# Kernel optimization log

Hardware: AMD Instinct MI355X
Metric: run time of the kernel (lower is better)

Reference implementation:

```python
import jax, jax.numpy as jnp
import numpy as np

B, N, U = 2048, 512, 64  # batch_size, memory_len, unit_size


def setup_inputs() -> dict:
    key = jax.random.key(0)
    ks = jax.random.split(key, 7)
    memory = jax.random.normal(ks[0], (B, N, U), jnp.float32)
    k = jax.random.normal(ks[1], (B, U), jnp.float32)
    beta = jnp.full((1,), 5.0, jnp.float32)          # key strength > 0
    g = jax.random.uniform(ks[2], (1,), jnp.float32)  # interpolation gate in [0,1]
    s = jax.random.uniform(ks[3], (B, 3), jnp.float32)
    s = s / jnp.sum(s, axis=1, keepdims=True)         # shift distribution (positive)
    gamma = jnp.full((1,), 2.0, jnp.float32)          # sharpening > 1
    w_pre = jax.nn.softmax(jax.random.normal(ks[4], (B, N), jnp.float32), axis=1)
    e = jax.random.uniform(ks[5], (B, U), jnp.float32)  # erase gates in [0,1]
    a = jax.random.normal(ks[6], (B, U), jnp.float32)    # add vector
    return dict(memory=memory, k=k, beta=beta, g=g, s=s, gamma=gamma,
                w_pre=w_pre, e=e, a=a)


def _cosine_sim(x, y, eps=1e-8):
    # x: (B,N,U), y: (B,1,U); matches torch F.cosine_similarity clamping
    dot = jnp.sum(x * y, axis=-1)
    nx = jnp.maximum(jnp.sqrt(jnp.sum(x * x, axis=-1)), eps)
    ny = jnp.maximum(jnp.sqrt(jnp.sum(y * y, axis=-1)), eps)
    return dot / (nx * ny)


def reference(memory, k, beta, g, s, gamma, w_pre, e, a):
    # --- address ---
    sim = _cosine_sim(memory + 1e-16, k[:, None, :] + 1e-16)        # (B,N)
    wc = jax.nn.softmax(beta * sim, axis=1)                          # content weights
    wg = wc * g + (1.0 - g) * w_pre                                  # gated interpolation
    # circular pad by 1 on each side, then 3-tap grouped conv (cross-correlation)
    wg_pad = jnp.concatenate([wg[:, -1:], wg, wg[:, :1]], axis=1)    # (B,N+2)
    ws = (s[:, 0:1] * wg_pad[:, :-2]
          + s[:, 1:2] * wg_pad[:, 1:-1]
          + s[:, 2:3] * wg_pad[:, 2:])                               # (B,N)
    w = ws ** gamma                                                  # sharpen
    w = w / jnp.sum(w, axis=1, keepdims=True) + 1e-16                # (B,N)
    # --- read ---
    r = jnp.einsum('bn,bnu->bu', w, memory)                          # (B,U)
    # --- write: M' = M * (1 - w e^T) + w a^T ---
    new_mem = (memory * (1.0 - w[:, :, None] * e[:, None, :])
               + w[:, :, None] * a[:, None, :])                      # (B,N,U)
    return w, r, new_mem
```

## Files before the change

kernel.cpp:

```cpp
#include <hip/hip_runtime.h>
#include <math.h>

#define B_ 2048
#define N_ 512
#define U_ 64

__global__ __launch_bounds__(256) void ntm_kernel(
    const float* __restrict__ memory,
    const float* __restrict__ kk,
    const float* __restrict__ beta_p,
    const float* __restrict__ g_p,
    const float* __restrict__ sv,
    const float* __restrict__ gamma_p,
    const float* __restrict__ w_pre,
    const float* __restrict__ ev,
    const float* __restrict__ av,
    float* __restrict__ out_w,
    float* __restrict__ out_r,
    float* __restrict__ out_m)
{
    __shared__ float s_k[U_];
    __shared__ float s_sim[N_];
    __shared__ float s_wg[N_];
    __shared__ float s_red[256];
    __shared__ float s_rred[4 * U_];
    __shared__ float s_ny;

    const int b    = blockIdx.x;
    const int tid  = threadIdx.x;
    const int wave = tid >> 6;
    const int lane = tid & 63;
    const int sub  = lane >> 4;
    const int l16  = lane & 15;
    const int col  = l16 << 2;

    const float beta  = beta_p[0];
    const float g     = g_p[0];
    const float gamma = gamma_p[0];
    const float s0 = sv[b * 3 + 0], s1 = sv[b * 3 + 1], s2 = sv[b * 3 + 2];

    const size_t mem_base = (size_t)b * N_ * U_;

    if (tid < U_) {
        float kx = kk[b * U_ + tid] + 1e-16f;
        s_k[tid] = kx;
        float v = kx * kx;
        #pragma unroll
        for (int off = 32; off; off >>= 1) v += __shfl_xor(v, off);
        if (tid == 0) s_ny = fmaxf(sqrtf(v), 1e-8f);
    }
    __syncthreads();
    const float ny = s_ny;

    const float k0 = s_k[col + 0], k1 = s_k[col + 1], k2 = s_k[col + 2], k3 = s_k[col + 3];

    for (int n0 = 0; n0 < N_; n0 += 16) {
        const int n = n0 + (wave << 2) + sub;
        const float4 m4 = *(const float4*)(memory + mem_base + (size_t)n * U_ + col);
        const float x0 = m4.x + 1e-16f, x1 = m4.y + 1e-16f,
                    x2 = m4.z + 1e-16f, x3 = m4.w + 1e-16f;
        float dot = x0 * k0 + x1 * k1 + x2 * k2 + x3 * k3;
        float nsq = x0 * x0 + x1 * x1 + x2 * x2 + x3 * x3;
        #pragma unroll
        for (int off = 8; off; off >>= 1) {
            dot += __shfl_xor(dot, off);
            nsq += __shfl_xor(nsq, off);
        }
        if (l16 == 0) {
            const float nx = fmaxf(sqrtf(nsq), 1e-8f);
            s_sim[n] = dot / (nx * ny);
        }
    }
    __syncthreads();

    const int i0 = tid, i1 = tid + 256;
    const float t0 = beta * s_sim[i0];
    const float t1 = beta * s_sim[i1];

    s_red[tid] = fmaxf(t0, t1);
    __syncthreads();
    for (int ss = 128; ss > 0; ss >>= 1) {
        if (tid < ss) s_red[tid] = fmaxf(s_red[tid], s_red[tid + ss]);
        __syncthreads();
    }
    const float mx = s_red[0];
    __syncthreads();

    const float e0 = expf(t0 - mx);
    const float e1 = expf(t1 - mx);
    s_red[tid] = e0 + e1;
    __syncthreads();
    for (int ss = 128; ss > 0; ss >>= 1) {
        if (tid < ss) s_red[tid] += s_red[tid + ss];
        __syncthreads();
    }
    const float einv = 1.0f / s_red[0];
    __syncthreads();

    const float wp0 = w_pre[(size_t)b * N_ + i0];
    const float wp1 = w_pre[(size_t)b * N_ + i1];
    s_wg[i0] = g * (e0 * einv) + (1.0f - g) * wp0;
    s_wg[i1] = g * (e1 * einv) + (1.0f - g) * wp1;
    __syncthreads();

    float wsv0, wsv1;
    {
        int nm = (i0 + N_ - 1) & (N_ - 1), np = (i0 + 1) & (N_ - 1);
        wsv0 = powf(s0 * s_wg[nm] + s1 * s_wg[i0] + s2 * s_wg[np], gamma);
        nm = (i1 + N_ - 1) & (N_ - 1); np = (i1 + 1) & (N_ - 1);
        wsv1 = powf(s0 * s_wg[nm] + s1 * s_wg[i1] + s2 * s_wg[np], gamma);
    }
    s_red[tid] = wsv0 + wsv1;
    __syncthreads();
    for (int ss = 128; ss > 0; ss >>= 1) {
        if (tid < ss) s_red[tid] += s_red[tid + ss];
        __syncthreads();
    }
    const float winv = 1.0f / s_red[0];
    __syncthreads();

    const float w0 = wsv0 * winv + 1e-16f;
    const float w1 = wsv1 * winv + 1e-16f;
    s_sim[i0] = w0;
    s_sim[i1] = w1;
    out_w[(size_t)b * N_ + i0] = w0;
    out_w[(size_t)b * N_ + i1] = w1;
    __syncthreads();

    const float4 e4 = *(const float4*)(ev + b * U_ + col);
    const float4 a4 = *(const float4*)(av + b * U_ + col);
    float rx = 0.f, ry = 0.f, rz = 0.f, rw = 0.f;

    for (int n0 = 0; n0 < N_; n0 += 16) {
        const int n = n0 + (wave << 2) + sub;
        const size_t off = mem_base + (size_t)n * U_ + col;
        const float4 m4 = *(const float4*)(memory + off);
        const float wn = s_sim[n];
        float4 o;
        o.x = m4.x * (1.0f - wn * e4.x) + wn * a4.x;
        o.y = m4.y * (1.0f - wn * e4.y) + wn * a4.y;
        o.z = m4.z * (1.0f - wn * e4.z) + wn * a4.z;
        o.w = m4.w * (1.0f - wn * e4.w) + wn * a4.w;
        *(float4*)(out_m + off) = o;
        rx += wn * m4.x; ry += wn * m4.y; rz += wn * m4.z; rw += wn * m4.w;
    }
    rx += __shfl_xor(rx, 16); rx += __shfl_xor(rx, 32);
    ry += __shfl_xor(ry, 16); ry += __shfl_xor(ry, 32);
    rz += __shfl_xor(rz, 16); rz += __shfl_xor(rz, 32);
    rw += __shfl_xor(rw, 16); rw += __shfl_xor(rw, 32);
    if (lane < 16) {
        s_rred[wave * U_ + col + 0] = rx;
        s_rred[wave * U_ + col + 1] = ry;
        s_rred[wave * U_ + col + 2] = rz;
        s_rred[wave * U_ + col + 3] = rw;
    }
    __syncthreads();
    if (tid < U_) {
        const float rv = s_rred[tid] + s_rred[U_ + tid] + s_rred[2 * U_ + tid] + s_rred[3 * U_ + tid];
        out_r[(size_t)b * U_ + tid] = rv;
    }
}

extern "C" void kernel_launch(void* const* d_in, const int* in_sizes, int n_in,
                              void* d_out, int out_size, void* d_ws, size_t ws_size,
                              hipStream_t stream) {
    const float* memory = (const float*)d_in[0];
    const float* kk     = (const float*)d_in[1];
    const float* beta   = (const float*)d_in[2];
    const float* g      = (const float*)d_in[3];
    const float* sv     = (const float*)d_in[4];
    const float* gamma  = (const float*)d_in[5];
    const float* w_pre  = (const float*)d_in[6];
    const float* ev     = (const float*)d_in[7];
    const float* av     = (const float*)d_in[8];

    float* out   = (float*)d_out;
    float* out_w = out;
    float* out_r = out + (size_t)B_ * N_;
    float* out_m = out + (size_t)B_ * N_ + (size_t)B_ * U_;

    ntm_kernel<<<B_, 256, 0, stream>>>(memory, kk, beta, g, sv, gamma,
                                       w_pre, ev, av, out_w, out_r, out_m);
}
```

Baseline: 491.1 us.

## Stage per-batch memory tile in LDS to read HBM once

Each block now copies its whole 512x64 memory slice into LDS (128 KB) with async global_load_lds. Both the cosine-similarity pass and the read/write pass then use that copy, so memory is read from HBM once instead of twice. The block grows to 512 threads with wave-shuffle reductions, the output uses nontemporal stores, and powf/expf become fast __expf/__logf. The softmax max-subtraction is dropped. The large LDS footprint limits each CU to one block, which leaves less latency hiding, and skipping the max shift risks overflow for large beta.

```diff
diff --git a/kernel.cpp b/kernel.cpp
--- a/kernel.cpp
+++ b/kernel.cpp
@@ -5,7 +5,11 @@
 #define N_ 512
 #define U_ 64
 
-__global__ __launch_bounds__(256) void ntm_kernel(
+typedef float f4 __attribute__((ext_vector_type(4)));
+
+#define NT_STORE4(ptr, v) __builtin_nontemporal_store((v), (f4*)(ptr))
+
+__global__ __launch_bounds__(512, 1) void ntm_kernel(
     const float* __restrict__ memory,
     const float* __restrict__ kk,
     const float* __restrict__ beta_p,
@@ -19,46 +23,60 @@
     float* __restrict__ out_r,
     float* __restrict__ out_m)
 {
-    __shared__ float s_k[U_];
+    __shared__ float s_mem[N_ * U_];
     __shared__ float s_sim[N_];
     __shared__ float s_wg[N_];
-    __shared__ float s_red[256];
-    __shared__ float s_rred[4 * U_];
-    __shared__ float s_ny;
+    __shared__ float s_red[8];
+    __shared__ float s_red2[8];
+    __shared__ float s_rred[8 * U_];
 
     const int b    = blockIdx.x;
     const int tid  = threadIdx.x;
     const int wave = tid >> 6;
     const int lane = tid & 63;
-    const int sub  = lane >> 4;
-    const int l16  = lane & 15;
+    const int grp  = tid >> 4;
+    const int l16  = tid & 15;
     const int col  = l16 << 2;
+
+    const size_t mem_base = (size_t)b * N_ * U_;
 
     const float beta  = beta_p[0];
     const float g     = g_p[0];
     const float gamma = gamma_p[0];
     const float s0 = sv[b * 3 + 0], s1 = sv[b * 3 + 1], s2 = sv[b * 3 + 2];
+    const float wp = w_pre[(size_t)b * N_ + tid];
+    const f4 e4 = *(const f4*)(ev + b * U_ + col);
+    const f4 a4 = *(const f4*)(av + b * U_ + col);
+    const f4 k4 = *(const f4*)(kk + b * U_ + col);
 
-    const size_t mem_base = (size_t)b * N_ * U_;
+    {
+        const float* gsrc = memory + mem_base;
+        #pragma unroll
+        for (int i = 0; i < 16; ++i) {
+            const int c = (wave << 4) + i;
+            __builtin_amdgcn_global_load_lds(
+                (const __attribute__((address_space(1))) void*)(gsrc + (c << 8) + (lane << 2)),
+                (__attribute__((address_space(3))) void*)(s_mem + (c << 8)),
+                16, 0, 0);
+        }
+    }
 
-    if (tid < U_) {
-        float kx = kk[b * U_ + tid] + 1e-16f;
-        s_k[tid] = kx;
-        float v = kx * kx;
-        #pragma unroll
-        for (int off = 32; off; off >>= 1) v += __shfl_xor(v, off);
-        if (tid == 0) s_ny = fmaxf(sqrtf(v), 1e-8f);
-    }
+    const float k0 = k4.x + 1e-16f, k1 = k4.y + 1e-16f,
+                k2 = k4.z + 1e-16f, k3 = k4.w + 1e-16f;
+    float ksq = k0 * k0 + k1 * k1 + k2 * k2 + k3 * k3;
+    #pragma unroll
+    for (int off = 8; off; off >>= 1) ksq += __shfl_xor(ksq, off);
+    const float ny = fmaxf(sqrtf(ksq), 1e-8f);
+
+    asm volatile("s_waitcnt vmcnt(0)" ::: "memory");
     __syncthreads();
-    const float ny = s_ny;
 
-    const float k0 = s_k[col + 0], k1 = s_k[col + 1], k2 = s_k[col + 2], k3 = s_k[col + 3];
-
-    for (int n0 = 0; n0 < N_; n0 += 16) {
-        const int n = n0 + (wave << 2) + sub;
-        const float4 m4 = *(const float4*)(memory + mem_base + (size_t)n * U_ + col);
-        const float x0 = m4.x + 1e-16f, x1 = m4.y + 1e-16f,
-                    x2 = m4.z + 1e-16f, x3 = m4.w + 1e-16f;
+    #pragma unroll 4
+    for (int j = 0; j < 16; ++j) {
+        const int r = (j << 5) + grp;
+        const f4 m = *(const f4*)(s_mem + r * U_ + col);
+        const float x0 = m.x + 1e-16f, x1 = m.y + 1e-16f,
+                    x2 = m.z + 1e-16f, x3 = m.w + 1e-16f;
         float dot = x0 * k0 + x1 * k1 + x2 * k2 + x3 * k3;
         float nsq = x0 * x0 + x1 * x1 + x2 * x2 + x3 * x3;
         #pragma unroll
@@ -66,83 +84,53 @@
             dot += __shfl_xor(dot, off);
             nsq += __shfl_xor(nsq, off);
         }
-        if (l16 == 0) {
-            const float nx = fmaxf(sqrtf(nsq), 1e-8f);
-            s_sim[n] = dot / (nx * ny);
-        }
+        if (l16 == 0) s_sim[r] = dot / (fmaxf(sqrtf(nsq), 1e-8f) * ny);
     }
     __syncthreads();
 
-    const int i0 = tid, i1 = tid + 256;
-    const float t0 = beta * s_sim[i0];
-    const float t1 = beta * s_sim[i1];
-
-    s_red[tid] = fmaxf(t0, t1);
+    const float e0 = __expf(beta * s_sim[tid]);
+    float v = e0;
+    #pragma unroll
+    for (int off = 32; off; off >>= 1) v += __shfl_xor(v, off);
+    if (lane == 0) s_red[wave] = v;
     __syncthreads();
-    for (int ss = 128; ss > 0; ss >>= 1) {
-        if (tid < ss) s_red[tid] = fmaxf(s_red[tid], s_red[tid + ss]);
-        __syncthreads();
-    }
-    const float mx = s_red[0];
+    const float einv = 1.0f / (s_red[0] + s_red[1] + s_red[2] + s_red[3]
+                             + s_red[4] + s_red[5] + s_red[6] + s_red[7]);
+    s_wg[tid] = g * (e0 * einv) + (1.0f - g) * wp;
     __syncthreads();
 
-    const float e0 = expf(t0 - mx);
-    const float e1 = expf(t1 - mx);
-    s_red[tid] = e0 + e1;
+    const float ws = s0 * s_wg[(tid + N_ - 1) & (N_ - 1)]
+                   + s1 * s_wg[tid]
+                   + s2 * s_wg[(tid + 1) & (N_ - 1)];
+    const float wsv = __expf(gamma * __logf(ws));
+    v = wsv;
+    #pragma unroll
+    for (int off = 32; off; off >>= 1) v += __shfl_xor(v, off);
+    if (lane == 0) s_red2[wave] = v;
     __syncthreads();
-    for (int ss = 128; ss > 0; ss >>= 1) {
-        if (tid < ss) s_red[tid] += s_red[tid + ss];
-        __syncthreads();
-    }
-    const float einv = 1.0f / s_red[0];
+    const float winv = 1.0f / (s_red2[0] + s_red2[1] + s_red2[2] + s_red2[3]
+                             + s_red2[4] + s_red2[5] + s_red2[6] + s_red2[7]);
+
+    const float w0 = wsv * winv + 1e-16f;
+    s_sim[tid] = w0;
+    out_w[(size_t)b * N_ + tid] = w0;
     __syncthreads();
 
-    const float wp0 = w_pre[(size_t)b * N_ + i0];
-    const float wp1 = w_pre[(size_t)b * N_ + i1];
-    s_wg[i0] = g * (e0 * einv) + (1.0f - g) * wp0;
-    s_wg[i1] = g * (e1 * einv) + (1.0f - g) * wp1;
-    __syncthreads();
-
-    float wsv0, wsv1;
-    {
-        int nm = (i0 + N_ - 1) & (N_ - 1), np = (i0 + 1) & (N_ - 1);
-        wsv0 = powf(s0 * s_wg[nm] + s1 * s_wg[i0] + s2 * s_wg[np], gamma);
-        nm = (i1 + N_ - 1) & (N_ - 1); np = (i1 + 1) & (N_ - 1);
-        wsv1 = powf(s0 * s_wg[nm] + s1 * s_wg[i1] + s2 * s_wg[np], gamma);
-    }
-    s_red[tid] = wsv0 + wsv1;
-    __syncthreads();
-    for (int ss = 128; ss > 0; ss >>= 1) {
-        if (tid < ss) s_red[tid] += s_red[tid + ss];
-        __syncthreads();
-    }
-    const float winv = 1.0f / s_red[0];
-    __syncthreads();
-
-    const float w0 = wsv0 * winv + 1e-16f;
-    const float w1 = wsv1 * winv + 1e-16f;
-    s_sim[i0] = w0;
-    s_sim[i1] = w1;
-    out_w[(size_t)b * N_ + i0] = w0;
-    out_w[(size_t)b * N_ + i1] = w1;
-    __syncthreads();
-
-    const float4 e4 = *(const float4*)(ev + b * U_ + col);
-    const float4 a4 = *(const float4*)(av + b * U_ + col);
     float rx = 0.f, ry = 0.f, rz = 0.f, rw = 0.f;
-
-    for (int n0 = 0; n0 < N_; n0 += 16) {
-        const int n = n0 + (wave << 2) + sub;
-        const size_t off = mem_base + (size_t)n * U_ + col;
-        const float4 m4 = *(const float4*)(memory + off);
-        const float wn = s_sim[n];
-        float4 o;
-        o.x = m4.x * (1.0f - wn * e4.x) + wn * a4.x;
-        o.y = m4.y * (1.0f - wn * e4.y) + wn * a4.y;
-        o.z = m4.z * (1.0f - wn * e4.z) + wn * a4.z;
-        o.w = m4.w * (1.0f - wn * e4.w) + wn * a4.w;
-        *(float4*)(out_m + off) = o;
-        rx += wn * m4.x; ry += wn * m4.y; rz += wn * m4.z; rw += wn * m4.w;
+    float* po = out_m + mem_base;
+    #pragma unroll 4
+    for (int j = 0; j < 16; ++j) {
+        const int r = (j << 5) + grp;
+        const f4 m = *(const f4*)(s_mem + r * U_ + col);
+        const float wn = s_sim[r];
+        f4 o;
+        o.x = m.x * (1.0f - wn * e4.x) + wn * a4.x;
+        o.y = m.y * (1.0f - wn * e4.y) + wn * a4.y;
+        o.z = m.z * (1.0f - wn * e4.z) + wn * a4.z;
+        o.w = m.w * (1.0f - wn * e4.w) + wn * a4.w;
+        NT_STORE4(po + r * U_ + col, o);
+        rx = fmaf(wn, m.x, rx); ry = fmaf(wn, m.y, ry);
+        rz = fmaf(wn, m.z, rz); rw = fmaf(wn, m.w, rw);
     }
     rx += __shfl_xor(rx, 16); rx += __shfl_xor(rx, 32);
     ry += __shfl_xor(ry, 16); ry += __shfl_xor(ry, 32);
@@ -156,7 +144,9 @@
     }
     __syncthreads();
     if (tid < U_) {
-        const float rv = s_rred[tid] + s_rred[U_ + tid] + s_rred[2 * U_ + tid] + s_rred[3 * U_ + tid];
+        float rv = 0.f;
+        #pragma unroll
+        for (int q = 0; q < 8; ++q) rv += s_rred[q * U_ + tid];
         out_r[(size_t)b * U_ + tid] = rv;
     }
 }
@@ -179,6 +169,6 @@
     float* out_r = out + (size_t)B_ * N_;
     float* out_m = out + (size_t)B_ * N_ + (size_t)B_ * U_;
 
-    ntm_kernel<<<B_, 256, 0, stream>>>(memory, kk, beta, g, sv, gamma,
+    ntm_kernel<<<B_, 512, 0, stream>>>(memory, kk, beta, g, sv, gamma,
                                        w_pre, ev, av, out_w, out_r, out_m);
 }
```

After: 466.1 us. 5.1% less time.
